# Performance work log

Measured on AMD Instinct MI355X. Metric: run time of the kernel, lower is better.

Reference implementation:

```python
import jax, jax.numpy as jnp
import numpy as np

L, B, S, H = 4, 2, 2048, 1024
NH, HD, FFN = 16, 64, 4096
EPS = 1e-5


def setup_inputs() -> dict:
    key = jax.random.key(0)
    ks = jax.random.split(key, 6)
    std = 0.02
    return {
        "hidden_states": jax.random.normal(ks[0], (B, S, H), jnp.float32),
        "ln1_g": jnp.ones((L, H), jnp.float32),
        "ln1_b": jnp.zeros((L, H), jnp.float32),
        "Wqkv": jax.random.normal(ks[1], (L, H, 3 * H), jnp.float32) * std,
        "Wproj": jax.random.normal(ks[2], (L, H, H), jnp.float32) * std,
        "ln2_g": jnp.ones((L, H), jnp.float32),
        "ln2_b": jnp.zeros((L, H), jnp.float32),
        "Wfc1": jax.random.normal(ks[3], (L, H, FFN), jnp.float32) * std,
        "Wfc2": jax.random.normal(ks[4], (L, FFN, H), jnp.float32) * std,
        "lnf_g": jnp.ones((H,), jnp.float32),
        "lnf_b": jnp.zeros((H,), jnp.float32),
    }


def _layernorm(x, g, b):
    mu = jnp.mean(x, axis=-1, keepdims=True)
    var = jnp.mean(jnp.square(x - mu), axis=-1, keepdims=True)
    return (x - mu) * jax.lax.rsqrt(var + EPS) * g + b


def _block_forward(x, ln1_g, ln1_b, Wqkv, Wproj, ln2_g, ln2_b, Wfc1, Wfc2, lnf_g, lnf_b):
    scale = HD ** -0.5
    causal = jnp.tril(jnp.ones((S, S), bool))  # [S, S]

    def layer(x, p):
        g1, b1, wqkv, wproj, g2, b2, wfc1, wfc2 = p
        # Attention sub-block (pre-norm)
        h = _layernorm(x, g1, b1)
        qkv = (h @ wqkv).reshape(B, S, 3, NH, HD)
        q, k, v = qkv[:, :, 0], qkv[:, :, 1], qkv[:, :, 2]  # [B,S,NH,HD]
        scores = jnp.einsum("bqhd,bkhd->bhqk", q, k) * scale
        scores = jnp.where(causal, scores, -jnp.inf)
        probs = jax.nn.softmax(scores, axis=-1)
        attn = jnp.einsum("bhqk,bkhd->bqhd", probs, v).reshape(B, S, H)
        x = x + attn @ wproj
        # FFN sub-block (pre-norm)
        h = _layernorm(x, g2, b2)
        h = jax.nn.gelu(h @ wfc1, approximate=False) @ wfc2
        return x + h, None

    x, _ = jax.lax.scan(layer, x, (ln1_g, ln1_b, Wqkv, Wproj, ln2_g, ln2_b, Wfc1, Wfc2))
    return _layernorm(x, lnf_g, lnf_b)


def reference(hidden_states, ln1_g, ln1_b, Wqkv, Wproj, ln2_g, ln2_b, Wfc1, Wfc2, lnf_g, lnf_b):
    return _block_forward(hidden_states, ln1_g, ln1_b, Wqkv, Wproj, ln2_g, ln2_b, Wfc1, Wfc2, lnf_g, lnf_b)
```

## Files before the change

### kernel.cpp

```cpp
#include <hip/hip_runtime.h>
#include <hip/hip_bf16.h>
#include <math.h>

#define LYRS 4
#define BB   2
#define SS   2048
#define HH   1024
#define NHD  16
#define HDD  64
#define FFN_ 4096
#define BS   (BB*SS)
#define EPS_ 1e-5f

typedef __attribute__((ext_vector_type(8))) __bf16 bf16x8;
typedef __attribute__((ext_vector_type(4))) __bf16 bf16x4;
typedef __attribute__((ext_vector_type(4))) float f32x4;
typedef __attribute__((address_space(1))) void* gas_t;
typedef __attribute__((address_space(3))) void* las_t;

__device__ inline void async16(void* lds, const void* g) {
    __builtin_amdgcn_global_load_lds((gas_t)g, (las_t)lds, 16, 0, 0);
}

__device__ inline void storev(float* p, float v) { *p = v; }
__device__ inline void storev(__hip_bfloat16* p, float v) { *p = __float2bfloat16(v); }

template <typename OutT>
__global__ void ln_k(const float* __restrict__ x, const float* __restrict__ g,
                     const float* __restrict__ b, OutT* __restrict__ y) {
    const int row = blockIdx.x;
    const int tid = threadIdx.x;
    const float* xr = x + (size_t)row * HH;

    float v[4];
    float s = 0.f, s2 = 0.f;
#pragma unroll
    for (int i = 0; i < 4; ++i) {
        v[i] = xr[tid + i * 256];
        s  += v[i];
        s2 += v[i] * v[i];
    }
#pragma unroll
    for (int o = 1; o < 64; o <<= 1) {
        s  += __shfl_xor(s,  o);
        s2 += __shfl_xor(s2, o);
    }
    __shared__ float sh[8];
    const int wave = tid >> 6, lane = tid & 63;
    if (lane == 0) { sh[wave] = s; sh[4 + wave] = s2; }
    __syncthreads();
    if (tid == 0) {
        float ts  = sh[0] + sh[1] + sh[2] + sh[3];
        float ts2 = sh[4] + sh[5] + sh[6] + sh[7];
        float mu  = ts * (1.f / HH);
        sh[0] = mu;
        sh[1] = ts2 * (1.f / HH) - mu * mu;
    }
    __syncthreads();
    const float mu   = sh[0];
    const float rstd = rsqrtf(sh[1] + EPS_);
#pragma unroll
    for (int i = 0; i < 4; ++i) {
        int c = tid + i * 256;
        storev(&y[(size_t)row * HH + c], (v[i] - mu) * rstd * g[c] + b[c]);
    }
}

__global__ __launch_bounds__(256) void transpose_cast(const float* __restrict__ W,
                                                      __hip_bfloat16* __restrict__ WT,
                                                      int K, int N) {
    __shared__ float t[32][33];
    const int n0 = blockIdx.x * 32, k0 = blockIdx.y * 32;
    const int tx = threadIdx.x & 31, ty8 = threadIdx.x >> 5;
#pragma unroll
    for (int i = 0; i < 4; ++i) {
        int k = ty8 + i * 8;
        t[k][tx] = W[(size_t)(k0 + k) * N + n0 + tx];
    }
    __syncthreads();
#pragma unroll
    for (int i = 0; i < 4; ++i) {
        int n = ty8 + i * 8;
        WT[(size_t)(n0 + n) * K + k0 + tx] = __float2bfloat16(t[tx][n]);
    }
}

template <bool GELU, bool RES, typename OutT>
__global__ __launch_bounds__(256) void gemm_bf16(
    const __hip_bfloat16* __restrict__ A,
    const __hip_bfloat16* __restrict__ BT,
    const float* __restrict__ R,
    OutT* __restrict__ C,
    int M, int N, int K)
{
    __shared__ unsigned short As[128 * 32];
    __shared__ unsigned short Bs[128 * 32];

    const int tid  = threadIdx.x;
    const int lane = tid & 63;
    const int wv   = tid >> 6;
    const int wy   = wv >> 1, wx = wv & 1;
    const int nby  = M >> 7;
    const int by   = blockIdx.x % nby;
    const int bx   = blockIdx.x / nby;
    const int row0 = by * 128;
    const int col0 = bx * 128;
    const int lm   = lane & 15;
    const int kq   = lane >> 4;

    const unsigned short* Ag = (const unsigned short*)A;
    const unsigned short* Bg = (const unsigned short*)BT;

    f32x4 acc[4][4] = {};

    for (int k0 = 0; k0 < K; k0 += 32) {
        __syncthreads();
#pragma unroll
        for (int it = 0; it < 2; ++it) {
            int li = it * 256 + tid;
            int r = li >> 2, c = (li & 3) << 3;
            async16(&As[li * 8], &Ag[(size_t)(row0 + r) * K + k0 + c]);
            async16(&Bs[li * 8], &Bg[(size_t)(col0 + r) * K + k0 + c]);
        }
        __syncthreads();

        bf16x8 af[4], bfr[4];
#pragma unroll
        for (int i = 0; i < 4; ++i)
            af[i] = *(const bf16x8*)&As[(wy * 64 + i * 16 + lm) * 32 + kq * 8];
#pragma unroll
        for (int j = 0; j < 4; ++j)
            bfr[j] = *(const bf16x8*)&Bs[(wx * 64 + j * 16 + lm) * 32 + kq * 8];
#pragma unroll
        for (int i = 0; i < 4; ++i)
#pragma unroll
            for (int j = 0; j < 4; ++j)
                acc[i][j] = __builtin_amdgcn_mfma_f32_16x16x32_bf16(
                    af[i], bfr[j], acc[i][j], 0, 0, 0);
    }

#pragma unroll
    for (int i = 0; i < 4; ++i) {
#pragma unroll
        for (int j = 0; j < 4; ++j) {
            int gc = col0 + wx * 64 + j * 16 + lm;
#pragma unroll
            for (int r = 0; r < 4; ++r) {
                int gr = row0 + wy * 64 + i * 16 + kq * 4 + r;
                float v = acc[i][j][r];
                if (RES)  v += R[(size_t)gr * N + gc];
                if (GELU) v = 0.5f * v * (1.0f + erff(v * 0.70710678118654752f));
                storev(&C[(size_t)gr * N + gc], v);
            }
        }
    }
}

__global__ __launch_bounds__(256) void attn_fa3(const __bf16* __restrict__ qkv,
                                                __bf16* __restrict__ out) {
    __shared__ __bf16 Ks[2][64 * 72];
    __shared__ __bf16 Vt[2][64 * 72];
    __shared__ __bf16 Ps[4][2][16 * 72];

    const int tid  = threadIdx.x;
    const int lane = tid & 63;
    const int w    = tid >> 6;
    const int lm   = lane & 15;
    const int kq   = lane >> 4;

    const int x  = blockIdx.x;
    const int bh = x & 31;
    const int h  = bh & 15;
    const int b  = bh >> 4;
    const int a  = (x >> 5) & 7;
    const int qt = (x & 256) ? (15 - a) : a;
    const int q0 = qt * 128;

    const size_t rs   = 3 * HH;
    const size_t base = (size_t)b * SS * rs + (size_t)h * HDD;

    const int krow0 = tid >> 3,        kc0 = (tid & 7) << 3;
    const int krow1 = (256 + tid) >> 3, kc1 = ((256 + tid) & 7) << 3;
    const int vkey  = tid & 63;
    const int vcb0  = (tid >> 6) << 3, vcb1 = ((256 + tid) >> 6) << 3;

    bf16x8 qf[2][2];
#pragma unroll
    for (int s = 0; s < 2; ++s)
#pragma unroll
        for (int kh = 0; kh < 2; ++kh) {
            bf16x8 t = *(const bf16x8*)&qkv[base +
                (size_t)(q0 + w * 32 + s * 16 + lm) * rs + kh * 32 + kq * 8];
#pragma unroll
            for (int j = 0; j < 8; ++j) t[j] = (__bf16)((float)t[j] * 0.125f);
            qf[s][kh] = t;
        }

    f32x4 ot[2][4] = {};
    float m_i[2] = {-INFINITY, -INFINITY};
    float l_i[2] = {0.f, 0.f};

    const int qmax_w = q0 + w * 32 + 31;
    const int ktmax  = (q0 + 127) >> 6;

    bf16x8 kr0, kr1, vr0, vr1;
    {
        const int k0 = 0;
        kr0 = *(const bf16x8*)&qkv[base + (size_t)(k0 + krow0) * rs + HH + kc0];
        kr1 = *(const bf16x8*)&qkv[base + (size_t)(k0 + krow1) * rs + HH + kc1];
        vr0 = *(const bf16x8*)&qkv[base + (size_t)(k0 + vkey) * rs + 2 * HH + vcb0];
        vr1 = *(const bf16x8*)&qkv[base + (size_t)(k0 + vkey) * rs + 2 * HH + vcb1];
        *(bf16x8*)&Ks[0][krow0 * 72 + kc0] = kr0;
        *(bf16x8*)&Ks[0][krow1 * 72 + kc1] = kr1;
#pragma unroll
        for (int j = 0; j < 8; ++j) Vt[0][(vcb0 + j) * 72 + vkey] = vr0[j];
#pragma unroll
        for (int j = 0; j < 8; ++j) Vt[0][(vcb1 + j) * 72 + vkey] = vr1[j];
    }
    __syncthreads();

    for (int kt = 0; kt <= ktmax; ++kt) {
        const int k0  = kt << 6;
        const int buf = kt & 1;

        if (kt < ktmax) {
            const int kn = k0 + 64;
            kr0 = *(const bf16x8*)&qkv[base + (size_t)(kn + krow0) * rs + HH + kc0];
            kr1 = *(const bf16x8*)&qkv[base + (size_t)(kn + krow1) * rs + HH + kc1];
            vr0 = *(const bf16x8*)&qkv[base + (size_t)(kn + vkey) * rs + 2 * HH + vcb0];
            vr1 = *(const bf16x8*)&qkv[base + (size_t)(kn + vkey) * rs + 2 * HH + vcb1];
        }

        if (k0 <= qmax_w) {
#pragma unroll
            for (int s = 0; s < 2; ++s) {
                f32x4 st[4] = {};
#pragma unroll
                for (int kh = 0; kh < 2; ++kh)
#pragma unroll
                    for (int m = 0; m < 4; ++m) {
                        bf16x8 kf = *(const bf16x8*)&Ks[buf][(m * 16 + lm) * 72 + kh * 32 + kq * 8];
                        st[m] = __builtin_amdgcn_mfma_f32_16x16x32_bf16(
                            kf, qf[s][kh], st[m], 0, 0, 0);
                    }

                const int qg = q0 + w * 32 + s * 16 + lm;
                if (k0 + 63 > q0 + w * 32 + s * 16) {
#pragma unroll
                    for (int m = 0; m < 4; ++m) {
                        int keyb = k0 + m * 16 + kq * 4;
#pragma unroll
                        for (int r = 0; r < 4; ++r)
                            if (keyb + r > qg) st[m][r] = -INFINITY;
                    }
                }

                float mloc = -INFINITY;
#pragma unroll
                for (int m = 0; m < 4; ++m)
#pragma unroll
                    for (int r = 0; r < 4; ++r) mloc = fmaxf(mloc, st[m][r]);
                mloc = fmaxf(mloc, __shfl_xor(mloc, 16));
                mloc = fmaxf(mloc, __shfl_xor(mloc, 32));
                float mn    = fmaxf(m_i[s], mloc);
                float alpha = __expf(m_i[s] - mn);
                m_i[s] = mn;

                float sum = 0.f;
#pragma unroll
                for (int m = 0; m < 4; ++m) {
                    bf16x4 pb;
#pragma unroll
                    for (int r = 0; r < 4; ++r) {
                        float p = __expf(st[m][r] - mn);
                        sum += p;
                        pb[r] = (__bf16)p;
                    }
                    *(bf16x4*)&Ps[w][s][lm * 72 + m * 16 + kq * 4] = pb;
                }
                sum += __shfl_xor(sum, 16);
                sum += __shfl_xor(sum, 32);
                l_i[s] = l_i[s] * alpha + sum;

#pragma unroll
                for (int dt = 0; dt < 4; ++dt) ot[s][dt] *= alpha;

#pragma unroll
                for (int kh = 0; kh < 2; ++kh) {
                    bf16x8 pf = *(const bf16x8*)&Ps[w][s][lm * 72 + kh * 32 + kq * 8];
#pragma unroll
                    for (int dt = 0; dt < 4; ++dt) {
                        bf16x8 vf = *(const bf16x8*)&Vt[buf][(dt * 16 + lm) * 72 + kh * 32 + kq * 8];
                        ot[s][dt] = __builtin_amdgcn_mfma_f32_16x16x32_bf16(
                            vf, pf, ot[s][dt], 0, 0, 0);
                    }
                }
            }
        }

        if (kt < ktmax) {
            const int nb = buf ^ 1;
            *(bf16x8*)&Ks[nb][krow0 * 72 + kc0] = kr0;
            *(bf16x8*)&Ks[nb][krow1 * 72 + kc1] = kr1;
#pragma unroll
            for (int j = 0; j < 8; ++j) Vt[nb][(vcb0 + j) * 72 + vkey] = vr0[j];
#pragma unroll
            for (int j = 0; j < 8; ++j) Vt[nb][(vcb1 + j) * 72 + vkey] = vr1[j];
            __syncthreads();
        }
    }

#pragma unroll
    for (int s = 0; s < 2; ++s) {
        float inv = 1.f / l_i[s];
        int qg = q0 + w * 32 + s * 16 + lm;
#pragma unroll
        for (int dt = 0; dt < 4; ++dt) {
            bf16x4 ob;
#pragma unroll
            for (int r = 0; r < 4; ++r) ob[r] = (__bf16)(ot[s][dt][r] * inv);
            *(bf16x4*)&out[(size_t)(b * SS + qg) * HH + h * HDD + dt * 16 + kq * 4] = ob;
        }
    }
}

extern "C" void kernel_launch(void* const* d_in, const int* in_sizes, int n_in,
                              void* d_out, int out_size, void* d_ws, size_t ws_size,
                              hipStream_t stream) {
    const float* hidden = (const float*)d_in[0];
    const float* ln1_g  = (const float*)d_in[1];
    const float* ln1_b  = (const float*)d_in[2];
    const float* Wqkv   = (const float*)d_in[3];
    const float* Wproj  = (const float*)d_in[4];
    const float* ln2_g  = (const float*)d_in[5];
    const float* ln2_b  = (const float*)d_in[6];
    const float* Wfc1   = (const float*)d_in[7];
    const float* Wfc2   = (const float*)d_in[8];
    const float* lnf_g  = (const float*)d_in[9];
    const float* lnf_b  = (const float*)d_in[10];

    float* x = (float*)d_out;

    char* p = (char*)d_ws;
    __hip_bfloat16* hbuf  = (__hip_bfloat16*)p; p += (size_t)BS * HH * 2;
    __hip_bfloat16* qkvb  = (__hip_bfloat16*)p; p += (size_t)BS * 3 * HH * 2;
    __hip_bfloat16* attnb = (__hip_bfloat16*)p; p += (size_t)BS * HH * 2;
    __hip_bfloat16* ffnb  = (__hip_bfloat16*)p; p += (size_t)BS * FFN_ * 2;
    __hip_bfloat16* wqkvT = (__hip_bfloat16*)p; p += (size_t)3 * HH * HH * 2;
    __hip_bfloat16* wprojT= (__hip_bfloat16*)p; p += (size_t)HH * HH * 2;
    __hip_bfloat16* wfc1T = (__hip_bfloat16*)p; p += (size_t)FFN_ * HH * 2;
    __hip_bfloat16* wfc2T = (__hip_bfloat16*)p; p += (size_t)HH * FFN_ * 2;

    hipMemcpyAsync(x, hidden, (size_t)BS * HH * sizeof(float),
                   hipMemcpyDeviceToDevice, stream);

    const int NBY = BS / 128;

    for (int lyr = 0; lyr < LYRS; ++lyr) {
        transpose_cast<<<dim3(3 * HH / 32, HH / 32), 256, 0, stream>>>(
            Wqkv + (size_t)lyr * HH * 3 * HH, wqkvT, HH, 3 * HH);
        transpose_cast<<<dim3(HH / 32, HH / 32), 256, 0, stream>>>(
            Wproj + (size_t)lyr * HH * HH, wprojT, HH, HH);
        transpose_cast<<<dim3(FFN_ / 32, HH / 32), 256, 0, stream>>>(
            Wfc1 + (size_t)lyr * HH * FFN_, wfc1T, HH, FFN_);
        transpose_cast<<<dim3(HH / 32, FFN_ / 32), 256, 0, stream>>>(
            Wfc2 + (size_t)lyr * FFN_ * HH, wfc2T, FFN_, HH);

        ln_k<__hip_bfloat16><<<BS, 256, 0, stream>>>(
            x, ln1_g + lyr * HH, ln1_b + lyr * HH, hbuf);
        gemm_bf16<false, false, __hip_bfloat16>
            <<<(3 * HH / 128) * NBY, 256, 0, stream>>>(
            hbuf, wqkvT, nullptr, qkvb, BS, 3 * HH, HH);
        attn_fa3<<<512, 256, 0, stream>>>((const __bf16*)qkvb, (__bf16*)attnb);
        gemm_bf16<false, true, float>
            <<<(HH / 128) * NBY, 256, 0, stream>>>(
            attnb, wprojT, x, x, BS, HH, HH);
        ln_k<__hip_bfloat16><<<BS, 256, 0, stream>>>(
            x, ln2_g + lyr * HH, ln2_b + lyr * HH, hbuf);
        gemm_bf16<true, false, __hip_bfloat16>
            <<<(FFN_ / 128) * NBY, 256, 0, stream>>>(
            hbuf, wfc1T, nullptr, ffnb, BS, FFN_, HH);
        gemm_bf16<false, true, float>
            <<<(HH / 128) * NBY, 256, 0, stream>>>(
            ffnb, wfc2T, x, x, BS, HH, FFN_);
    }
    ln_k<float><<<BS, 256, 0, stream>>>(x, lnf_g, lnf_b, x);
}
```

Before: 1.409 ms.

## Double-buffer GEMM LDS staging and split-K the FC2 GEMM with atomic accumulation

The GEMM kernel now uses two LDS buffers, so the async global-to-LDS load for the next K step is issued before the MFMAs of the current step. That drops one barrier per iteration and lets memory latency overlap with compute. The FC2 GEMM (K=4096, only 256 tiles) is split into two K slices whose partial sums are atomically added straight into the residual x, which doubles the block count to fill more CUs. The cost is extra float atomic traffic and a non-deterministic summation order. The LDS footprint also doubles, which may lower occupancy.

```diff
diff --git a/kernel.cpp b/kernel.cpp
--- a/kernel.cpp
+++ b/kernel.cpp
@@ -85,7 +85,7 @@
     }
 }
 
-template <bool GELU, bool RES, typename OutT>
+template <bool GELU, bool RES, int SPLITK, typename OutT>
 __global__ __launch_bounds__(256) void gemm_bf16(
     const __hip_bfloat16* __restrict__ A,
     const __hip_bfloat16* __restrict__ BT,
@@ -93,50 +93,70 @@
     OutT* __restrict__ C,
     int M, int N, int K)
 {
-    __shared__ unsigned short As[128 * 32];
-    __shared__ unsigned short Bs[128 * 32];
+    __shared__ unsigned short As[2][128 * 32];
+    __shared__ unsigned short Bs[2][128 * 32];
 
     const int tid  = threadIdx.x;
     const int lane = tid & 63;
     const int wv   = tid >> 6;
     const int wy   = wv >> 1, wx = wv & 1;
     const int nby  = M >> 7;
-    const int by   = blockIdx.x % nby;
-    const int bx   = blockIdx.x / nby;
+    const int tiles = nby * (N >> 7);
+    const int ks   = blockIdx.x / tiles;
+    const int rem  = blockIdx.x % tiles;
+    const int by   = rem % nby;
+    const int bx   = rem / nby;
     const int row0 = by * 128;
     const int col0 = bx * 128;
     const int lm   = lane & 15;
     const int kq   = lane >> 4;
 
+    const int Kslice = K / SPLITK;
+    const int kbeg   = ks * Kslice;
+    const int nsteps = Kslice >> 5;
+
     const unsigned short* Ag = (const unsigned short*)A;
     const unsigned short* Bg = (const unsigned short*)BT;
 
+    const int li0 = tid, li1 = 256 + tid;
+    const int r0 = li0 >> 2, c0 = (li0 & 3) << 3;
+    const int r1 = li1 >> 2, c1 = (li1 & 3) << 3;
+    const unsigned short* Ag0 = Ag + (size_t)(row0 + r0) * K + c0;
+    const unsigned short* Ag1 = Ag + (size_t)(row0 + r1) * K + c1;
+    const unsigned short* Bg0 = Bg + (size_t)(col0 + r0) * K + c0;
+    const unsigned short* Bg1 = Bg + (size_t)(col0 + r1) * K + c1;
+
+    auto stage = [&](int buf, int k) {
+        async16(&As[buf][li0 * 8], Ag0 + k);
+        async16(&As[buf][li1 * 8], Ag1 + k);
+        async16(&Bs[buf][li0 * 8], Bg0 + k);
+        async16(&Bs[buf][li1 * 8], Bg1 + k);
+    };
+
     f32x4 acc[4][4] = {};
 
-    for (int k0 = 0; k0 < K; k0 += 32) {
-        __syncthreads();
-#pragma unroll
-        for (int it = 0; it < 2; ++it) {
-            int li = it * 256 + tid;
-            int r = li >> 2, c = (li & 3) << 3;
-            async16(&As[li * 8], &Ag[(size_t)(row0 + r) * K + k0 + c]);
-            async16(&Bs[li * 8], &Bg[(size_t)(col0 + r) * K + k0 + c]);
-        }
-        __syncthreads();
+    stage(0, kbeg);
+    __syncthreads();
+
+    for (int s = 0; s < nsteps; ++s) {
+        const int buf = s & 1;
+        if (s + 1 < nsteps) stage(buf ^ 1, kbeg + ((s + 1) << 5));
 
         bf16x8 af[4], bfr[4];
 #pragma unroll
         for (int i = 0; i < 4; ++i)
-            af[i] = *(const bf16x8*)&As[(wy * 64 + i * 16 + lm) * 32 + kq * 8];
+            af[i] = *(const bf16x8*)&As[buf][(wy * 64 + i * 16 + lm) * 32 + kq * 8];
 #pragma unroll
         for (int j = 0; j < 4; ++j)
-            bfr[j] = *(const bf16x8*)&Bs[(wx * 64 + j * 16 + lm) * 32 + kq * 8];
+            bfr[j] = *(const bf16x8*)&Bs[buf][(wx * 64 + j * 16 + lm) * 32 + kq * 8];
 #pragma unroll
         for (int i = 0; i < 4; ++i)
 #pragma unroll
             for (int j = 0; j < 4; ++j)
                 acc[i][j] = __builtin_amdgcn_mfma_f32_16x16x32_bf16(
                     af[i], bfr[j], acc[i][j], 0, 0, 0);
+
+        __syncthreads();
     }
 
 #pragma unroll
@@ -148,9 +168,13 @@
             for (int r = 0; r < 4; ++r) {
                 int gr = row0 + wy * 64 + i * 16 + kq * 4 + r;
                 float v = acc[i][j][r];
-                if (RES)  v += R[(size_t)gr * N + gc];
-                if (GELU) v = 0.5f * v * (1.0f + erff(v * 0.70710678118654752f));
-                storev(&C[(size_t)gr * N + gc], v);
+                if constexpr (SPLITK > 1) {
+                    atomicAdd((float*)&C[(size_t)gr * N + gc], v);
+                } else {
+                    if (RES)  v += R[(size_t)gr * N + gc];
+                    if (GELU) v = 0.5f * v * (1.0f + erff(v * 0.70710678118654752f));
+                    storev(&C[(size_t)gr * N + gc], v);
+                }
             }
         }
     }
@@ -368,21 +392,21 @@
 
         ln_k<__hip_bfloat16><<<BS, 256, 0, stream>>>(
             x, ln1_g + lyr * HH, ln1_b + lyr * HH, hbuf);
-        gemm_bf16<false, false, __hip_bfloat16>
+        gemm_bf16<false, false, 1, __hip_bfloat16>
             <<<(3 * HH / 128) * NBY, 256, 0, stream>>>(
             hbuf, wqkvT, nullptr, qkvb, BS, 3 * HH, HH);
         attn_fa3<<<512, 256, 0, stream>>>((const __bf16*)qkvb, (__bf16*)attnb);
-        gemm_bf16<false, true, float>
+        gemm_bf16<false, true, 1, float>
             <<<(HH / 128) * NBY, 256, 0, stream>>>(
             attnb, wprojT, x, x, BS, HH, HH);
         ln_k<__hip_bfloat16><<<BS, 256, 0, stream>>>(
             x, ln2_g + lyr * HH, ln2_b + lyr * HH, hbuf);
-        gemm_bf16<true, false, __hip_bfloat16>
+        gemm_bf16<true, false, 1, __hip_bfloat16>
             <<<(FFN_ / 128) * NBY, 256, 0, stream>>>(
             hbuf, wfc1T, nullptr, ffnb, BS, FFN_, HH);
-        gemm_bf16<false, true, float>
-            <<<(HH / 128) * NBY, 256, 0, stream>>>(
-            ffnb, wfc2T, x, x, BS, HH, FFN_);
+        gemm_bf16<false, false, 2, float>
+            <<<(HH / 128) * NBY * 2, 256, 0, stream>>>(
+            ffnb, wfc2T, nullptr, x, BS, HH, FFN_);
     }
     ln_k<float><<<BS, 256, 0, stream>>>(x, lnf_g, lnf_b, x);
 }
```

Result: faster. 1.277 ms (-9.4%).
